# Performance work log

Measured on AMD Instinct MI355X. Metric: run time of the kernel, lower is better.

The kernel has to match this reference:

```python
import jax, jax.numpy as jnp
import numpy as np

H = 32          # num attention heads
D = 128         # head dim
HID = 4096      # hidden size
MIN_R = 1.0     # compress_ratio_min
MAX_R = 3.0     # compress_ratio_max
BASE = 10000.0  # rope_theta


def rotate_half(x):
    x1, x2 = jnp.split(x, 2, axis=-1)
    return jnp.concatenate([-x2, x1], axis=-1)


def ms_poe_cos_sin(seq_len):
    # Per-head compressed positions: t_h = arange(S) / ratio_h
    inv_freq = 1.0 / (BASE ** (jnp.arange(0, D, 2, dtype=jnp.float32) / D))   # [D/2]
    ratio = MIN_R + (MAX_R - MIN_R) * (jnp.arange(H, dtype=jnp.float32) / H)  # [H]
    t = jnp.arange(seq_len, dtype=jnp.float32)[None, :] / ratio[:, None]      # [H,S]
    freqs = t[:, :, None] * inv_freq[None, None, :]                           # [H,S,D/2]
    emb = jnp.concatenate([freqs, freqs], axis=-1)                            # [H,S,D]
    return jnp.cos(emb), jnp.sin(emb)


def setup_inputs() -> dict:
    key = jax.random.key(0)
    ks = jax.random.split(key, 5)
    B, S = 1, 2048
    scale = 0.02
    return {
        "hidden_states": jax.random.normal(ks[0], (B, S, HID), dtype=jnp.float32),
        "position_ids": jnp.broadcast_to(jnp.arange(S, dtype=jnp.int64 if jax.config.jax_enable_x64 else jnp.int32), (B, S)),
        "wq": jax.random.normal(ks[1], (HID, HID), dtype=jnp.float32) * scale,
        "wk": jax.random.normal(ks[2], (HID, HID), dtype=jnp.float32) * scale,
        "wv": jax.random.normal(ks[3], (HID, HID), dtype=jnp.float32) * scale,
        "wo": jax.random.normal(ks[4], (HID, HID), dtype=jnp.float32) * scale,
    }


def reference(hidden_states, position_ids, wq, wk, wv, wo):
    B, S, _ = hidden_states.shape
    dtype = hidden_states.dtype

    # QKV projections (torch Linear: y = x @ W.T), split into heads -> [B,H,S,D]
    q = (hidden_states @ wq.T).reshape(B, S, H, D).transpose(0, 2, 1, 3)
    k = (hidden_states @ wk.T).reshape(B, S, H, D).transpose(0, 2, 1, 3)
    v = (hidden_states @ wv.T).reshape(B, S, H, D).transpose(0, 2, 1, 3)

    # Per-head scaled rotary embedding; head_type='normal' -> reversed head order
    cos, sin = ms_poe_cos_sin(S)                 # [H,S,D]
    order = H - jnp.arange(H) - 1
    cos, sin = cos[order], sin[order]

    # cos[:, position_ids] -> [H,B,S,D] -> transpose(0,1) -> [B,H,S,D]
    cos_p = jnp.transpose(cos[:, position_ids], (1, 0, 2, 3)).astype(dtype)
    sin_p = jnp.transpose(sin[:, position_ids], (1, 0, 2, 3)).astype(dtype)

    q = q * cos_p + rotate_half(q) * sin_p
    # num_key_value_groups == 1 -> sample_rotary_emb is identity; same cos/sin for k
    k = k * cos_p + rotate_half(k) * sin_p

    # Causal softmax attention (eager, as in original)
    scores = jnp.einsum("bhqd,bhkd->bhqk", q, k) / jnp.sqrt(jnp.asarray(D, dtype))
    neg = jnp.finfo(dtype).min
    causal = jnp.where(jnp.tril(jnp.ones((S, S), dtype=bool)), 0.0, neg).astype(dtype)
    scores = scores + causal[None, None]
    attn = jax.nn.softmax(scores, axis=-1)
    out = jnp.einsum("bhqk,bhkd->bhqd", attn, v)  # [B,H,S,D]

    out = out.transpose(0, 2, 1, 3).reshape(B, S, HID)
    return out @ wo.T
```

## Files before the change

kernel.cpp:

```cpp
#include <hip/hip_runtime.h>
#include <math.h>

#define HIDDEN 4096
#define NHEADS 32
#define HEADDIM 128

__global__ __launch_bounds__(256)
void gemm_nt(const float* __restrict__ A, const float* __restrict__ B,
             float* __restrict__ C, int M, int N, int K) {
  __shared__ float As[16][128];
  __shared__ float Bs[16][128];
  const int tid = threadIdx.x;
  const int bm = blockIdx.y * 128;
  const int bn = blockIdx.x * 128;
  const int ty = tid >> 4;
  const int tx = tid & 15;
  const int lrow = tid >> 1;
  const int lkq  = (tid & 1) * 4;

  float acc[8][8];
#pragma unroll
  for (int i = 0; i < 8; ++i)
#pragma unroll
    for (int j = 0; j < 8; ++j) acc[i][j] = 0.f;

  const float* Ap = A + (size_t)(bm + lrow) * K + lkq;
  const float* Bp = B + (size_t)(bn + lrow) * K + lkq;

  for (int kt = 0; kt < K; kt += 16) {
    float4 a0 = *(const float4*)(Ap + kt);
    float4 a1 = *(const float4*)(Ap + kt + 8);
    float4 b0 = *(const float4*)(Bp + kt);
    float4 b1 = *(const float4*)(Bp + kt + 8);
    __syncthreads();
    As[lkq + 0][lrow] = a0.x; As[lkq + 1][lrow] = a0.y;
    As[lkq + 2][lrow] = a0.z; As[lkq + 3][lrow] = a0.w;
    As[lkq + 8][lrow] = a1.x; As[lkq + 9][lrow] = a1.y;
    As[lkq +10][lrow] = a1.z; As[lkq +11][lrow] = a1.w;
    Bs[lkq + 0][lrow] = b0.x; Bs[lkq + 1][lrow] = b0.y;
    Bs[lkq + 2][lrow] = b0.z; Bs[lkq + 3][lrow] = b0.w;
    Bs[lkq + 8][lrow] = b1.x; Bs[lkq + 9][lrow] = b1.y;
    Bs[lkq +10][lrow] = b1.z; Bs[lkq +11][lrow] = b1.w;
    __syncthreads();
#pragma unroll
    for (int k = 0; k < 16; ++k) {
      float a[8], b[8];
      *(float4*)&a[0] = *(const float4*)&As[k][ty * 8];
      *(float4*)&a[4] = *(const float4*)&As[k][ty * 8 + 4];
      *(float4*)&b[0] = *(const float4*)&Bs[k][tx * 8];
      *(float4*)&b[4] = *(const float4*)&Bs[k][tx * 8 + 4];
#pragma unroll
      for (int i = 0; i < 8; ++i)
#pragma unroll
        for (int j = 0; j < 8; ++j)
          acc[i][j] = fmaf(a[i], b[j], acc[i][j]);
    }
  }
  float* Cp = C + (size_t)(bm + ty * 8) * N + bn + tx * 8;
#pragma unroll
  for (int i = 0; i < 8; ++i) {
    *(float4*)(Cp + (size_t)i * N)     = *(float4*)&acc[i][0];
    *(float4*)(Cp + (size_t)i * N + 4) = *(float4*)&acc[i][4];
  }
}

__global__ __launch_bounds__(256)
void rope_kernel(float* __restrict__ Q, float* __restrict__ Kc,
                 const int* __restrict__ pos_ids, int S) {
  const int row = blockIdx.x * 4 + (threadIdx.x >> 6);
  const int j = threadIdx.x & 63;
  const int s = row >> 5;
  const int h = row & 31;
  const int pos = pos_ids[s];
  const int hr = NHEADS - 1 - h;
  const float ratio = 1.0f + 2.0f * ((float)hr / 32.0f);
  const float t = (float)pos / ratio;
  const float inv = (float)exp(-0.143911568312127875 * (double)j);
  const float ang = t * inv;
  float sn, cs;
  sincosf(ang, &sn, &cs);
  const size_t base = (size_t)s * HIDDEN + (size_t)h * HEADDIM + j;
  const float q0 = Q[base], q1 = Q[base + 64];
  Q[base]      = q0 * cs - q1 * sn;
  Q[base + 64] = q1 * cs + q0 * sn;
  const float k0 = Kc[base], k1 = Kc[base + 64];
  Kc[base]      = k0 * cs - k1 * sn;
  Kc[base + 64] = k1 * cs + k0 * sn;
}

__global__ __launch_bounds__(256)
void attn_kernel(const float* __restrict__ Q, const float* __restrict__ K,
                 const float* __restrict__ V, float* __restrict__ O, int S) {
  __shared__ float Ks[32][160];
  __shared__ float Vs[32][160];
  const int h = blockIdx.y;
  const int nqb = S >> 5;
  const int qb = nqb - 1 - blockIdx.x;
  const int tid = threadIdx.x;
  const int wave = tid >> 6;
  const int lane = tid & 63;
  const int r = lane >> 3;
  const int c = lane & 7;
  const int qrow = qb * 32 + wave * 8 + r;
  const float scale = 0.08838834764831845f;

  float qf[16];
  {
    const float* qp = Q + (size_t)qrow * HIDDEN + h * HEADDIM + c * 16;
#pragma unroll
    for (int i = 0; i < 4; ++i)
      *(float4*)&qf[i * 4] = *(const float4*)(qp + i * 4);
  }
  float o[16];
#pragma unroll
  for (int i = 0; i < 16; ++i) o[i] = 0.f;
  float m = -INFINITY, l = 0.f;

  const int strow = tid >> 3;
  const int stc = tid & 7;
  const int ntiles = qb + 1;
  for (int t0 = 0; t0 < ntiles; ++t0) {
    const int kb = t0 * 32;
    __syncthreads();
    {
      const float* kg = K + (size_t)(kb + strow) * HIDDEN + h * HEADDIM;
      const float* vg = V + (size_t)(kb + strow) * HIDDEN + h * HEADDIM;
#pragma unroll
      for (int jj = 0; jj < 4; ++jj) {
        const int cc = stc + jj * 8;
        float4 kv = *(const float4*)(kg + cc * 4);
        float4 vv = *(const float4*)(vg + cc * 4);
        const int off = (cc >> 2) * 20 + (cc & 3) * 4;
        *(float4*)&Ks[strow][off] = kv;
        *(float4*)&Vs[strow][off] = vv;
      }
    }
    __syncthreads();

    float sv[32];
#pragma unroll
    for (int kk = 0; kk < 32; ++kk) {
      const float* kr = &Ks[kk][c * 20];
      float kv[16];
#pragma unroll
      for (int i = 0; i < 4; ++i)
        *(float4*)&kv[i * 4] = *(const float4*)(kr + i * 4);
      float d0 = 0.f, d1 = 0.f, d2 = 0.f, d3 = 0.f;
#pragma unroll
      for (int i = 0; i < 4; ++i) {
        d0 = fmaf(qf[i],      kv[i],      d0);
        d1 = fmaf(qf[4 + i],  kv[4 + i],  d1);
        d2 = fmaf(qf[8 + i],  kv[8 + i],  d2);
        d3 = fmaf(qf[12 + i], kv[12 + i], d3);
      }
      float d = (d0 + d1) + (d2 + d3);
      d += __shfl_xor(d, 1);
      d += __shfl_xor(d, 2);
      d += __shfl_xor(d, 4);
      sv[kk] = (kb + kk <= qrow) ? d * scale : -INFINITY;
    }
    float tmax = -INFINITY;
#pragma unroll
    for (int kk = 0; kk < 32; ++kk) tmax = fmaxf(tmax, sv[kk]);
    const float mnew = fmaxf(m, tmax);
    const float corr = __expf(m - mnew);
#pragma unroll
    for (int i = 0; i < 16; ++i) o[i] *= corr;
    float psum = 0.f;
#pragma unroll
    for (int kk = 0; kk < 32; ++kk) {
      const float p = __expf(sv[kk] - mnew);
      psum += p;
      const float* vr = &Vs[kk][c * 20];
      float vvv[16];
#pragma unroll
      for (int i = 0; i < 4; ++i)
        *(float4*)&vvv[i * 4] = *(const float4*)(vr + i * 4);
#pragma unroll
      for (int i = 0; i < 16; ++i) o[i] = fmaf(p, vvv[i], o[i]);
    }
    l = l * corr + psum;
    m = mnew;
  }
  const float invl = 1.0f / l;
  float* op = O + (size_t)qrow * HIDDEN + h * HEADDIM + c * 16;
#pragma unroll
  for (int i = 0; i < 4; ++i) {
    float4 ov;
    ov.x = o[i * 4 + 0] * invl;
    ov.y = o[i * 4 + 1] * invl;
    ov.z = o[i * 4 + 2] * invl;
    ov.w = o[i * 4 + 3] * invl;
    *(float4*)(op + i * 4) = ov;
  }
}

extern "C" void kernel_launch(void* const* d_in, const int* in_sizes, int n_in,
                              void* d_out, int out_size, void* d_ws, size_t ws_size,
                              hipStream_t stream) {
  const float* hs  = (const float*)d_in[0];
  const int*   pos = (const int*)d_in[1];
  const float* wq  = (const float*)d_in[2];
  const float* wk  = (const float*)d_in[3];
  const float* wv  = (const float*)d_in[4];
  const float* wo  = (const float*)d_in[5];
  float* out = (float*)d_out;

  const int S = in_sizes[0] / HIDDEN;
  const size_t plane = (size_t)S * HIDDEN;

  float* q  = (float*)d_ws;
  float* k  = q + plane;
  float* ao = k + plane;
  float* v  = out;

  dim3 gblk(256);
  dim3 ggrid(HIDDEN / 128, S / 128);
  gemm_nt<<<ggrid, gblk, 0, stream>>>(hs, wq, q, S, HIDDEN, HIDDEN);
  gemm_nt<<<ggrid, gblk, 0, stream>>>(hs, wk, k, S, HIDDEN, HIDDEN);
  gemm_nt<<<ggrid, gblk, 0, stream>>>(hs, wv, v, S, HIDDEN, HIDDEN);

  rope_kernel<<<(S * NHEADS) / 4, 256, 0, stream>>>(q, k, pos, S);

  attn_kernel<<<dim3(S / 32, NHEADS), 256, 0, stream>>>(q, k, v, ao, S);

  gemm_nt<<<ggrid, gblk, 0, stream>>>(ao, wo, out, S, HIDDEN, HIDDEN);
}
```

Measured before the change: 4.914 ms.

## Use split-bf16x3 MFMA GEMMs and pair causal q-blocks in attention

New measurement: 4.729 ms. 1.04x faster.

```diff
diff --git a/kernel.cpp b/kernel.cpp
--- a/kernel.cpp
+++ b/kernel.cpp
@@ -4,6 +4,123 @@
 #define HIDDEN 4096
 #define NHEADS 32
 #define HEADDIM 128
+
+typedef __attribute__((ext_vector_type(8))) short bf16x8;
+typedef __attribute__((ext_vector_type(4))) float f32x4;
+
+#define GLL(g, l) __builtin_amdgcn_global_load_lds( \
+    (const __attribute__((address_space(1))) void*)(g), \
+    (__attribute__((address_space(3))) void*)(l), 16, 0, 0)
+
+__device__ __forceinline__ unsigned short f2bf(float f) {
+  unsigned int u = __float_as_uint(f);
+  unsigned int r = (u + 0x7FFFu + ((u >> 16) & 1u)) >> 16;
+  return (unsigned short)r;
+}
+__device__ __forceinline__ float bf2f(unsigned short h) {
+  return __uint_as_float(((unsigned int)h) << 16);
+}
+
+__global__ __launch_bounds__(256)
+void split_bf16(const float* __restrict__ X, unsigned short* __restrict__ H,
+                unsigned short* __restrict__ L) {
+  const int i = blockIdx.x * 256 + threadIdx.x;
+  float4 v = ((const float4*)X)[i];
+  ushort4 h, lo;
+  const float* vf = (const float*)&v;
+  unsigned short* hp = (unsigned short*)&h;
+  unsigned short* lp = (unsigned short*)&lo;
+#pragma unroll
+  for (int j = 0; j < 4; ++j) {
+    float f = vf[j];
+    unsigned short hb = f2bf(f);
+    hp[j] = hb;
+    lp[j] = f2bf(f - bf2f(hb));
+  }
+  ((ushort4*)H)[i] = h;
+  ((ushort4*)L)[i] = lo;
+}
+
+__global__ __launch_bounds__(256)
+void gemm_bf16x3(const unsigned short* __restrict__ Ahi, const unsigned short* __restrict__ Alo,
+                 const unsigned short* __restrict__ Bhi, const unsigned short* __restrict__ Blo,
+                 float* __restrict__ C, int M, int N, int K) {
+  __shared__ unsigned short lds[4 * 4096];
+  const int tid = threadIdx.x;
+  const int bm = blockIdx.y * 128;
+  const int bn = blockIdx.x * 128;
+  const int w = tid >> 6, l = tid & 63;
+  const int wr = (w >> 1) * 64, wc = (w & 1) * 64;
+  const int lr = l & 15, lc = l >> 4;
+
+  f32x4 acc[4][4];
+#pragma unroll
+  for (int m = 0; m < 4; ++m)
+#pragma unroll
+    for (int n = 0; n < 4; ++n) acc[m][n] = (f32x4){0.f, 0.f, 0.f, 0.f};
+
+  const int p0 = tid, p1 = tid + 256;
+  const int r0 = p0 >> 2, c0 = (p0 & 3) ^ (r0 & 3);
+  const int r1 = p1 >> 2, c1 = (p1 & 3) ^ (r1 & 3);
+  const size_t a0 = (size_t)(bm + r0) * K + c0 * 8;
+  const size_t a1 = (size_t)(bm + r1) * K + c1 * 8;
+  const size_t b0 = (size_t)(bn + r0) * K + c0 * 8;
+  const size_t b1 = (size_t)(bn + r1) * K + c1 * 8;
+  unsigned short* lp0 = &lds[p0 * 8];
+  unsigned short* lp1 = &lds[p1 * 8];
+
+  const int fa = (lc ^ (lr & 3)) * 8;
+  int aoff[4], boff[4];
+#pragma unroll
+  for (int m = 0; m < 4; ++m) aoff[m] = (wr + m * 16 + lr) * 32 + fa;
+#pragma unroll
+  for (int n = 0; n < 4; ++n) boff[n] = (wc + n * 16 + lr) * 32 + fa;
+
+  for (int kt = 0; kt < K; kt += 32) {
+    GLL(Ahi + a0 + kt, lp0);
+    GLL(Ahi + a1 + kt, lp1);
+    GLL(Alo + a0 + kt, lp0 + 4096);
+    GLL(Alo + a1 + kt, lp1 + 4096);
+    GLL(Bhi + b0 + kt, lp0 + 8192);
+    GLL(Bhi + b1 + kt, lp1 + 8192);
+    GLL(Blo + b0 + kt, lp0 + 12288);
+    GLL(Blo + b1 + kt, lp1 + 12288);
+    __syncthreads();
+
+    bf16x8 ah[4], al[4], bh[4], bl[4];
+#pragma unroll
+    for (int m = 0; m < 4; ++m) {
+      ah[m] = *(const bf16x8*)&lds[aoff[m]];
+      al[m] = *(const bf16x8*)&lds[4096 + aoff[m]];
+    }
+#pragma unroll
+    for (int n = 0; n < 4; ++n) {
+      bh[n] = *(const bf16x8*)&lds[8192 + boff[n]];
+      bl[n] = *(const bf16x8*)&lds[12288 + boff[n]];
+    }
+#pragma unroll
+    for (int m = 0; m < 4; ++m)
+#pragma unroll
+      for (int n = 0; n < 4; ++n) {
+        acc[m][n] = __builtin_amdgcn_mfma_f32_16x16x32_bf16(ah[m], bh[n], acc[m][n], 0, 0, 0);
+        acc[m][n] = __builtin_amdgcn_mfma_f32_16x16x32_bf16(ah[m], bl[n], acc[m][n], 0, 0, 0);
+        acc[m][n] = __builtin_amdgcn_mfma_f32_16x16x32_bf16(al[m], bh[n], acc[m][n], 0, 0, 0);
+      }
+    __syncthreads();
+  }
+
+#pragma unroll
+  for (int m = 0; m < 4; ++m) {
+    const int row0 = bm + wr + m * 16 + lc * 4;
+#pragma unroll
+    for (int n = 0; n < 4; ++n) {
+      const int col = bn + wc + n * 16 + lr;
+      float* cp = C + (size_t)row0 * N + col;
+#pragma unroll
+      for (int j = 0; j < 4; ++j) cp[(size_t)j * N] = acc[m][n][j];
+    }
+  }
+}
 
 __global__ __launch_bounds__(256)
 void gemm_nt(const float* __restrict__ A, const float* __restrict__ B,
@@ -16,7 +133,7 @@
   const int ty = tid >> 4;
   const int tx = tid & 15;
   const int lrow = tid >> 1;
-  const int lkq  = (tid & 1) * 4;
+  const int lkq = (tid & 1) * 4;
 
   float acc[8][8];
 #pragma unroll
@@ -52,14 +169,13 @@
 #pragma unroll
       for (int i = 0; i < 8; ++i)
 #pragma unroll
-        for (int j = 0; j < 8; ++j)
-          acc[i][j] = fmaf(a[i], b[j], acc[i][j]);
+        for (int j = 0; j < 8; ++j) acc[i][j] = fmaf(a[i], b[j], acc[i][j]);
     }
   }
   float* Cp = C + (size_t)(bm + ty * 8) * N + bn + tx * 8;
 #pragma unroll
   for (int i = 0; i < 8; ++i) {
-    *(float4*)(Cp + (size_t)i * N)     = *(float4*)&acc[i][0];
+    *(float4*)(Cp + (size_t)i * N) = *(float4*)&acc[i][0];
     *(float4*)(Cp + (size_t)i * N + 4) = *(float4*)&acc[i][4];
   }
 }
@@ -81,148 +197,188 @@
   sincosf(ang, &sn, &cs);
   const size_t base = (size_t)s * HIDDEN + (size_t)h * HEADDIM + j;
   const float q0 = Q[base], q1 = Q[base + 64];
-  Q[base]      = q0 * cs - q1 * sn;
+  Q[base] = q0 * cs - q1 * sn;
   Q[base + 64] = q1 * cs + q0 * sn;
   const float k0 = Kc[base], k1 = Kc[base + 64];
-  Kc[base]      = k0 * cs - k1 * sn;
+  Kc[base] = k0 * cs - k1 * sn;
   Kc[base + 64] = k1 * cs + k0 * sn;
 }
 
 __global__ __launch_bounds__(256)
 void attn_kernel(const float* __restrict__ Q, const float* __restrict__ K,
                  const float* __restrict__ V, float* __restrict__ O, int S) {
-  __shared__ float Ks[32][160];
-  __shared__ float Vs[32][160];
+  __shared__ float Ks[32 * 128];
+  __shared__ float Vs[32 * 128];
   const int h = blockIdx.y;
   const int nqb = S >> 5;
-  const int qb = nqb - 1 - blockIdx.x;
   const int tid = threadIdx.x;
-  const int wave = tid >> 6;
-  const int lane = tid & 63;
-  const int r = lane >> 3;
-  const int c = lane & 7;
-  const int qrow = qb * 32 + wave * 8 + r;
+  const int wave = tid >> 6, lane = tid & 63;
+  const int r = lane >> 3, c = lane & 7;
+  const int strow = tid >> 3, stc = tid & 7;
   const float scale = 0.08838834764831845f;
 
-  float qf[16];
-  {
-    const float* qp = Q + (size_t)qrow * HIDDEN + h * HEADDIM + c * 16;
+  for (int half = 0; half < 2; ++half) {
+    const int qb = half ? (nqb - 1 - (int)blockIdx.x) : (int)blockIdx.x;
+    const int qrow = qb * 32 + wave * 8 + r;
+    const float* qp = Q + (size_t)qrow * HIDDEN + h * HEADDIM;
+    float qf[16];
 #pragma unroll
     for (int i = 0; i < 4; ++i)
-      *(float4*)&qf[i * 4] = *(const float4*)(qp + i * 4);
-  }
-  float o[16];
-#pragma unroll
-  for (int i = 0; i < 16; ++i) o[i] = 0.f;
-  float m = -INFINITY, l = 0.f;
-
-  const int strow = tid >> 3;
-  const int stc = tid & 7;
-  const int ntiles = qb + 1;
-  for (int t0 = 0; t0 < ntiles; ++t0) {
-    const int kb = t0 * 32;
-    __syncthreads();
-    {
-      const float* kg = K + (size_t)(kb + strow) * HIDDEN + h * HEADDIM;
-      const float* vg = V + (size_t)(kb + strow) * HIDDEN + h * HEADDIM;
+      *(float4*)&qf[i * 4] = *(const float4*)(qp + c * 4 + 32 * i);
+    float o[16];
+#pragma unroll
+    for (int i = 0; i < 16; ++i) o[i] = 0.f;
+    float m = -INFINITY, l = 0.f;
+    const int ntiles = qb + 1;
+
+    const float* kg = K + (size_t)strow * HIDDEN + h * HEADDIM;
+    const float* vg = V + (size_t)strow * HIDDEN + h * HEADDIM;
+    float4 kreg[4], vreg[4];
+#pragma unroll
+    for (int jj = 0; jj < 4; ++jj) {
+      kreg[jj] = *(const float4*)(kg + (stc + jj * 8) * 4);
+      vreg[jj] = *(const float4*)(vg + (stc + jj * 8) * 4);
+    }
+    for (int t = 0; t < ntiles; ++t) {
+      __syncthreads();
 #pragma unroll
       for (int jj = 0; jj < 4; ++jj) {
-        const int cc = stc + jj * 8;
-        float4 kv = *(const float4*)(kg + cc * 4);
-        float4 vv = *(const float4*)(vg + cc * 4);
-        const int off = (cc >> 2) * 20 + (cc & 3) * 4;
-        *(float4*)&Ks[strow][off] = kv;
-        *(float4*)&Vs[strow][off] = vv;
-      }
-    }
-    __syncthreads();
-
-    float sv[32];
-#pragma unroll
-    for (int kk = 0; kk < 32; ++kk) {
-      const float* kr = &Ks[kk][c * 20];
-      float kv[16];
-#pragma unroll
-      for (int i = 0; i < 4; ++i)
-        *(float4*)&kv[i * 4] = *(const float4*)(kr + i * 4);
-      float d0 = 0.f, d1 = 0.f, d2 = 0.f, d3 = 0.f;
-#pragma unroll
-      for (int i = 0; i < 4; ++i) {
-        d0 = fmaf(qf[i],      kv[i],      d0);
-        d1 = fmaf(qf[4 + i],  kv[4 + i],  d1);
-        d2 = fmaf(qf[8 + i],  kv[8 + i],  d2);
-        d3 = fmaf(qf[12 + i], kv[12 + i], d3);
-      }
-      float d = (d0 + d1) + (d2 + d3);
-      d += __shfl_xor(d, 1);
-      d += __shfl_xor(d, 2);
-      d += __shfl_xor(d, 4);
-      sv[kk] = (kb + kk <= qrow) ? d * scale : -INFINITY;
-    }
-    float tmax = -INFINITY;
-#pragma unroll
-    for (int kk = 0; kk < 32; ++kk) tmax = fmaxf(tmax, sv[kk]);
-    const float mnew = fmaxf(m, tmax);
-    const float corr = __expf(m - mnew);
-#pragma unroll
-    for (int i = 0; i < 16; ++i) o[i] *= corr;
-    float psum = 0.f;
-#pragma unroll
-    for (int kk = 0; kk < 32; ++kk) {
-      const float p = __expf(sv[kk] - mnew);
-      psum += p;
-      const float* vr = &Vs[kk][c * 20];
-      float vvv[16];
-#pragma unroll
-      for (int i = 0; i < 4; ++i)
-        *(float4*)&vvv[i * 4] = *(const float4*)(vr + i * 4);
-#pragma unroll
-      for (int i = 0; i < 16; ++i) o[i] = fmaf(p, vvv[i], o[i]);
-    }
-    l = l * corr + psum;
-    m = mnew;
-  }
-  const float invl = 1.0f / l;
-  float* op = O + (size_t)qrow * HIDDEN + h * HEADDIM + c * 16;
-#pragma unroll
-  for (int i = 0; i < 4; ++i) {
-    float4 ov;
-    ov.x = o[i * 4 + 0] * invl;
-    ov.y = o[i * 4 + 1] * invl;
-    ov.z = o[i * 4 + 2] * invl;
-    ov.w = o[i * 4 + 3] * invl;
-    *(float4*)(op + i * 4) = ov;
+        *(float4*)&Ks[strow * 128 + (stc + jj * 8) * 4] = kreg[jj];
+        *(float4*)&Vs[strow * 128 + (stc + jj * 8) * 4] = vreg[jj];
+      }
+      if (t + 1 < ntiles) {
+        const float* kg2 = kg + (size_t)(t + 1) * 32 * HIDDEN;
+        const float* vg2 = vg + (size_t)(t + 1) * 32 * HIDDEN;
+#pragma unroll
+        for (int jj = 0; jj < 4; ++jj) {
+          kreg[jj] = *(const float4*)(kg2 + (stc + jj * 8) * 4);
+          vreg[jj] = *(const float4*)(vg2 + (stc + jj * 8) * 4);
+        }
+      }
+      __syncthreads();
+
+      const int kb = t * 32;
+      float sv[32];
+#pragma unroll
+      for (int kk = 0; kk < 32; ++kk) {
+        const float* kr = &Ks[kk * 128 + c * 4];
+        float kv[16];
+#pragma unroll
+        for (int i = 0; i < 4; ++i)
+          *(float4*)&kv[i * 4] = *(const float4*)(kr + 32 * i);
+        float d0 = 0.f, d1 = 0.f, d2 = 0.f, d3 = 0.f;
+#pragma unroll
+        for (int i = 0; i < 4; ++i) {
+          d0 = fmaf(qf[i], kv[i], d0);
+          d1 = fmaf(qf[4 + i], kv[4 + i], d1);
+          d2 = fmaf(qf[8 + i], kv[8 + i], d2);
+          d3 = fmaf(qf[12 + i], kv[12 + i], d3);
+        }
+        float d = (d0 + d1) + (d2 + d3);
+        d += __shfl_xor(d, 1);
+        d += __shfl_xor(d, 2);
+        d += __shfl_xor(d, 4);
+        sv[kk] = (kb + kk <= qrow) ? d * scale : -INFINITY;
+      }
+      float tmax = -INFINITY;
+#pragma unroll
+      for (int kk = 0; kk < 32; ++kk) tmax = fmaxf(tmax, sv[kk]);
+      const float mnew = fmaxf(m, tmax);
+      const float corr = __expf(m - mnew);
+#pragma unroll
+      for (int i = 0; i < 16; ++i) o[i] *= corr;
+      float psum = 0.f;
+#pragma unroll
+      for (int kk = 0; kk < 32; ++kk) {
+        const float p = __expf(sv[kk] - mnew);
+        psum += p;
+        const float* vr = &Vs[kk * 128 + c * 4];
+        float vv[16];
+#pragma unroll
+        for (int i = 0; i < 4; ++i)
+          *(float4*)&vv[i * 4] = *(const float4*)(vr + 32 * i);
+#pragma unroll
+        for (int i = 0; i < 16; ++i) o[i] = fmaf(p, vv[i], o[i]);
+      }
+      l = l * corr + psum;
+      m = mnew;
+    }
+    const float invl = 1.0f / l;
+    float* op = O + (size_t)qrow * HIDDEN + h * HEADDIM + c * 4;
+#pragma unroll
+    for (int i = 0; i < 4; ++i) {
+      float4 ov;
+      ov.x = o[i * 4 + 0] * invl;
+      ov.y = o[i * 4 + 1] * invl;
+      ov.z = o[i * 4 + 2] * invl;
+      ov.w = o[i * 4 + 3] * invl;
+      *(float4*)(op + 32 * i) = ov;
+    }
   }
 }
 
 extern "C" void kernel_launch(void* const* d_in, const int* in_sizes, int n_in,
                               void* d_out, int out_size, void* d_ws, size_t ws_size,
                               hipStream_t stream) {
-  const float* hs  = (const float*)d_in[0];
-  const int*   pos = (const int*)d_in[1];
-  const float* wq  = (const float*)d_in[2];
-  const float* wk  = (const float*)d_in[3];
-  const float* wv  = (const float*)d_in[4];
-  const float* wo  = (const float*)d_in[5];
+  const float* hs = (const float*)d_in[0];
+  const int* pos = (const int*)d_in[1];
+  const float* wq = (const float*)d_in[2];
+  const float* wk = (const float*)d_in[3];
+  const float* wv = (const float*)d_in[4];
+  const float* wo = (const float*)d_in[5];
   float* out = (float*)d_out;
 
   const int S = in_sizes[0] / HIDDEN;
-  const size_t plane = (size_t)S * HIDDEN;
-
-  float* q  = (float*)d_ws;
-  float* k  = q + plane;
-  float* ao = k + plane;
-  float* v  = out;
-
-  dim3 gblk(256);
-  dim3 ggrid(HIDDEN / 128, S / 128);
-  gemm_nt<<<ggrid, gblk, 0, stream>>>(hs, wq, q, S, HIDDEN, HIDDEN);
-  gemm_nt<<<ggrid, gblk, 0, stream>>>(hs, wk, k, S, HIDDEN, HIDDEN);
-  gemm_nt<<<ggrid, gblk, 0, stream>>>(hs, wv, v, S, HIDDEN, HIDDEN);
-
-  rope_kernel<<<(S * NHEADS) / 4, 256, 0, stream>>>(q, k, pos, S);
-
-  attn_kernel<<<dim3(S / 32, NHEADS), 256, 0, stream>>>(q, k, v, ao, S);
-
-  gemm_nt<<<ggrid, gblk, 0, stream>>>(ao, wo, out, S, HIDDEN, HIDDEN);
-}
+  const size_t planeF = (size_t)S * HIDDEN * sizeof(float);
+  const size_t planeH = (size_t)S * HIDDEN * sizeof(short);
+  const size_t wplaneH = (size_t)HIDDEN * HIDDEN * sizeof(short);
+  const size_t needed = 3 * planeF + 4 * planeH + 8 * wplaneH;
+
+  char* wp = (char*)d_ws;
+  float* q = (float*)wp;   wp += planeF;
+  float* k = (float*)wp;   wp += planeF;
+  float* ao = (float*)wp;  wp += planeF;
+  float* v = out;
+
+  dim3 mg(HIDDEN / 128, S / 128);
+  const int nh = S * HIDDEN;
+  const int nw = HIDDEN * HIDDEN;
+
+  if (ws_size >= needed) {
+    unsigned short* hs_hi = (unsigned short*)wp;  wp += planeH;
+    unsigned short* hs_lo = (unsigned short*)wp;  wp += planeH;
+    unsigned short* ao_hi = (unsigned short*)wp;  wp += planeH;
+    unsigned short* ao_lo = (unsigned short*)wp;  wp += planeH;
+    unsigned short* wqh = (unsigned short*)wp;  wp += wplaneH;
+    unsigned short* wql = (unsigned short*)wp;  wp += wplaneH;
+    unsigned short* wkh = (unsigned short*)wp;  wp += wplaneH;
+    unsigned short* wkl = (unsigned short*)wp;  wp += wplaneH;
+    unsigned short* wvh = (unsigned short*)wp;  wp += wplaneH;
+    unsigned short* wvl = (unsigned short*)wp;  wp += wplaneH;
+    unsigned short* woh = (unsigned short*)wp;  wp += wplaneH;
+    unsigned short* wol = (unsigned short*)wp;  wp += wplaneH;
+
+    split_bf16<<<nh / 1024, 256, 0, stream>>>(hs, hs_hi, hs_lo);
+    split_bf16<<<nw / 1024, 256, 0, stream>>>(wq, wqh, wql);
+    split_bf16<<<nw / 1024, 256, 0, stream>>>(wk, wkh, wkl);
+    split_bf16<<<nw / 1024, 256, 0, stream>>>(wv, wvh, wvl);
+    split_bf16<<<nw / 1024, 256, 0, stream>>>(wo, woh, wol);
+
+    gemm_bf16x3<<<mg, 256, 0, stream>>>(hs_hi, hs_lo, wqh, wql, q, S, HIDDEN, HIDDEN);
+    gemm_bf16x3<<<mg, 256, 0, stream>>>(hs_hi, hs_lo, wkh, wkl, k, S, HIDDEN, HIDDEN);
+    gemm_bf16x3<<<mg, 256, 0, stream>>>(hs_hi, hs_lo, wvh, wvl, v, S, HIDDEN, HIDDEN);
+
+    rope_kernel<<<(S * NHEADS) / 4, 256, 0, stream>>>(q, k, pos, S);
+    attn_kernel<<<dim3(S / 64, NHEADS), 256, 0, stream>>>(q, k, v, ao, S);
+
+    split_bf16<<<nh / 1024, 256, 0, stream>>>(ao, ao_hi, ao_lo);
+    gemm_bf16x3<<<mg, 256, 0, stream>>>(ao_hi, ao_lo, woh, wol, out, S, HIDDEN, HIDDEN);
+  } else {
+    gemm_nt<<<mg, 256, 0, stream>>>(hs, wq, q, S, HIDDEN, HIDDEN);
+    gemm_nt<<<mg, 256, 0, stream>>>(hs, wk, k, S, HIDDEN, HIDDEN);
+    gemm_nt<<<mg, 256, 0, stream>>>(hs, wv, v, S, HIDDEN, HIDDEN);
+    rope_kernel<<<(S * NHEADS) / 4, 256, 0, stream>>>(q, k, pos, S);
+    attn_kernel<<<dim3(S / 64, NHEADS), 256, 0, stream>>>(q, k, v, ao, S);
+    gemm_nt<<<mg, 256, 0, stream>>>(ao, wo, out, S, HIDDEN, HIDDEN);
+  }
+}
```
